# Performance work log

Hardware: AMD Instinct MI355X
Metric: run time of the kernel (lower is better)

The kernel has to match this reference:

```python
import jax, jax.numpy as jnp
import numpy as np

C = 64            # x_channel (d_model)
D = 2 * C         # d_inner (expand=2)
N = C // 2        # d_state
K = 4             # scan directions
R = -(-C // 16)   # dt_rank = ceil(d_model/16)
Bsz, H, W = 2, 48, 48
EPS = 1e-5


def setup_inputs() -> dict:
    key = jax.random.key(0)
    ks = jax.random.split(key, 8)
    g = lambda k, shp, s: jax.random.normal(k, shp, dtype=jnp.float32) * s
    return {
        "fufea1": g(ks[0], (Bsz, C, H, W), 1.0),
        "ln_g": jnp.ones((C,), jnp.float32),
        "ln_b": jnp.zeros((C,), jnp.float32),
        "in_proj_w": g(ks[1], (2 * D, C), C ** -0.5),
        "conv_w": g(ks[2], (D, 1, 3, 3), 1.0 / 3.0),   # depthwise 3x3
        "conv_b": g(ks[3], (D,), 0.02),
        "x_proj_w": g(ks[4], (K, R + 2 * N, D), D ** -0.5),
        "dt_w": g(ks[5], (K, D, R), R ** -0.5),
        "dt_b": g(ks[6], (K, D), 0.1),
        "A_logs": jnp.log(jnp.tile(jnp.arange(1, N + 1, dtype=jnp.float32), (K, D, 1))),  # S4D-real init
        "Ds": jnp.ones((K, D), jnp.float32),
        "out_ln_g": jnp.ones((D,), jnp.float32),
        "out_ln_b": jnp.zeros((D,), jnp.float32),
        "out_proj_w": g(ks[7], (C, D), D ** -0.5),
    }


def _layernorm(x, g, b):
    mu = x.mean(-1, keepdims=True)
    var = ((x - mu) ** 2).mean(-1, keepdims=True)
    return (x - mu) * jax.lax.rsqrt(var + EPS) * g + b


def reference(fufea1, ln_g, ln_b, in_proj_w, conv_w, conv_b, x_proj_w,
              dt_w, dt_b, A_logs, Ds, out_ln_g, out_ln_b, out_proj_w):
    B, Cc, Hh, Ww = fufea1.shape
    L = Hh * Ww
    # pre-LN (over channels, channels-last)
    xn = _layernorm(fufea1.transpose(0, 2, 3, 1), ln_g, ln_b)          # (B,H,W,C)
    # SS2D: in_proj -> split x,z
    xz = xn @ in_proj_w.T                                               # (B,H,W,2D)
    x, z = jnp.split(xz, 2, axis=-1)
    x = x.transpose(0, 3, 1, 2)                                         # (B,D,H,W)
    x = jax.lax.conv_general_dilated(x, conv_w, (1, 1), "SAME",
                                     feature_group_count=D,
                                     dimension_numbers=("NCHW", "OIHW", "NCHW"))
    x = jax.nn.silu(x + conv_b[None, :, None, None])
    # 4-direction sequences: row-major, col-major, and their reverses
    x_hw = x.reshape(B, D, L)
    x_wh = x.transpose(0, 1, 3, 2).reshape(B, D, L)
    xs = jnp.stack([x_hw, x_wh], axis=1)                                # (B,2,D,L)
    xs = jnp.concatenate([xs, jnp.flip(xs, axis=-1)], axis=1)           # (B,K,D,L)
    # per-direction projections of dt, B, C
    x_dbl = jnp.einsum("bkdl,kcd->bkcl", xs, x_proj_w)
    dts, Bs, Cs = jnp.split(x_dbl, [R, R + N], axis=2)                  # (B,K,R,L),(B,K,N,L),(B,K,N,L)
    dts = jnp.einsum("bkrl,kdr->bkdl", dts, dt_w)
    delta = jax.nn.softplus(dts + dt_b[None, :, :, None])               # (B,K,D,L)
    A = -jnp.exp(A_logs)                                                # (K,D,N)
    # selective scan over L; carry h: (B,K,D,N)
    u_l = xs.transpose(3, 0, 1, 2)                                      # (L,B,K,D)
    dt_l = delta.transpose(3, 0, 1, 2)
    B_l = Bs.transpose(3, 0, 1, 2)                                      # (L,B,K,N)
    C_l = Cs.transpose(3, 0, 1, 2)

    def step(h, inp):
        u_t, d_t, b_t, c_t = inp
        dA = jnp.exp(d_t[..., None] * A)                                # (B,K,D,N)
        h = dA * h + (d_t * u_t)[..., None] * b_t[:, :, None, :]
        y = jnp.einsum("bkdn,bkn->bkd", h, c_t)
        return h, y

    h0 = jnp.zeros((B, K, D, N), xs.dtype)
    _, ys = jax.lax.scan(step, h0, (u_l, dt_l, B_l, C_l))               # ys: (L,B,K,D)
    out_y = ys.transpose(1, 2, 3, 0) + Ds[None, :, :, None] * xs        # (B,K,D,L)
    # merge the 4 directions back to row-major hw order
    inv_y = jnp.flip(out_y[:, 2:4], axis=-1)                            # (B,2,D,L)
    wh = lambda t: t.reshape(B, D, Ww, Hh).transpose(0, 1, 3, 2).reshape(B, D, L)
    y = out_y[:, 0] + inv_y[:, 0] + wh(out_y[:, 1]) + wh(inv_y[:, 1])   # (B,D,L)
    y = y.transpose(0, 2, 1).reshape(B, Hh, Ww, D)
    y = _layernorm(y, out_ln_g, out_ln_b) * jax.nn.silu(z)
    out = (y @ out_proj_w.T).transpose(0, 3, 1, 2) + fufea1             # residual add
    return out
```

## Files before the change

kernel.cpp:

```cpp
#include <hip/hip_runtime.h>

#define Cc 64
#define Dd 128
#define Nn 32
#define Kk 4
#define Rr 4
#define Bb 2
#define Hh 48
#define Ww 48
#define Ll 2304
#define EPSf 1e-5f
#define LCc 144

#if __has_builtin(__builtin_amdgcn_exp2f)
#define EXP2F __builtin_amdgcn_exp2f
#else
#define EXP2F exp2f
#endif

__device__ __forceinline__ float wsum64(float v) {
  v += __shfl_xor(v, 32);
  v += __shfl_xor(v, 16);
  v += __shfl_xor(v, 8);
  v += __shfl_xor(v, 4);
  v += __shfl_xor(v, 2);
  v += __shfl_xor(v, 1);
  return v;
}

__global__ __launch_bounds__(256) void k1_ln_inproj(
    const float* __restrict__ x, const float* __restrict__ g,
    const float* __restrict__ bta, const float* __restrict__ Wp,
    float* __restrict__ xin, float* __restrict__ zb)
{
  __shared__ float xS[16][65];
  __shared__ float xnS[16][64];
  __shared__ float xaS[128][17];
  const int tid = threadIdx.x;
  const int wv = tid >> 6, lane = tid & 63;
  const int pbase = blockIdx.x * 16;
  const int b = pbase / Ll;
  const int lbase = pbase % Ll;
  {
    const int c = tid >> 2, li0 = (tid & 3) * 4;
    const float4 v4 = *(const float4*)&x[(b * Cc + c) * Ll + lbase + li0];
    xS[li0 + 0][c] = v4.x;
    xS[li0 + 1][c] = v4.y;
    xS[li0 + 2][c] = v4.z;
    xS[li0 + 3][c] = v4.w;
  }
  __syncthreads();
  const float gv = g[lane], bv = bta[lane];
  for (int pi = 0; pi < 4; ++pi) {
    const int p = wv * 4 + pi;
    const float v = xS[p][lane];
    const float mu = wsum64(v) * (1.0f / 64.0f);
    const float dv = v - mu;
    const float var = wsum64(dv * dv) * (1.0f / 64.0f);
    const float rs = rsqrtf(var + EPSf);
    xnS[p][lane] = dv * rs * gv + bv;
  }
  __syncthreads();
  float acc[4][4];
  #pragma unroll
  for (int pi = 0; pi < 4; ++pi)
    #pragma unroll
    for (int m = 0; m < 4; ++m) acc[pi][m] = 0.f;
  const float4* W4 = (const float4*)Wp;
  #pragma unroll 4
  for (int c4 = 0; c4 < 16; ++c4) {
    float4 xn4[4];
    #pragma unroll
    for (int pi = 0; pi < 4; ++pi)
      xn4[pi] = ((const float4*)xnS[wv * 4 + pi])[c4];
    #pragma unroll
    for (int m = 0; m < 4; ++m) {
      const float4 w4 = W4[(lane + 64 * m) * 16 + c4];
      #pragma unroll
      for (int pi = 0; pi < 4; ++pi)
        acc[pi][m] += xn4[pi].x * w4.x + xn4[pi].y * w4.y +
                      xn4[pi].z * w4.z + xn4[pi].w * w4.w;
    }
  }
  #pragma unroll
  for (int pi = 0; pi < 4; ++pi) {
    const int l = lbase + wv * 4 + pi;
    zb[(b * Ll + l) * Dd + lane]      = acc[pi][2];
    zb[(b * Ll + l) * Dd + lane + 64] = acc[pi][3];
    xaS[lane][wv * 4 + pi]      = acc[pi][0];
    xaS[lane + 64][wv * 4 + pi] = acc[pi][1];
  }
  __syncthreads();
  const int d = tid >> 1, off = (tid & 1) * 8;
  float* dst = &xin[(b * Dd + d) * Ll + lbase + off];
  #pragma unroll
  for (int i = 0; i < 8; ++i) dst[i] = xaS[d][off + i];
}

__global__ __launch_bounds__(512) void k3_proj(
    const float* __restrict__ xin, const float* __restrict__ cw,
    const float* __restrict__ cb, const float* __restrict__ xpw,
    const float* __restrict__ dtw, const float* __restrict__ dtb,
    float* __restrict__ xc, float2* __restrict__ dd2,
    float* __restrict__ Bm, float* __restrict__ Cm)
{
  __shared__ float xinS[128][30];
  __shared__ float xvS[8][132];
  __shared__ float dtsS[8][16];
  const int t = threadIdx.x;
  const int pb = blockIdx.x * 8;
  const int b = pb / Ll;
  const int lb = pb % Ll;
  const int h0 = lb / Ww, w0 = lb % Ww;
  for (int i = t; i < 3840; i += 512) {
    const int d = i / 30, j = i % 30;
    const int r = j / 10, c = j % 10;
    const int hh = h0 + r - 1, ww = w0 + c - 1;
    float v = 0.f;
    if (hh >= 0 && hh < Hh && ww >= 0 && ww < Ww)
      v = xin[(b * Dd + d) * Ll + hh * Ww + ww];
    xinS[d][j] = v;
  }
  __syncthreads();
  for (int i = t; i < 1024; i += 512) {
    const int pi = i >> 7, d = i & 127;
    float acc = cb[d];
    #pragma unroll
    for (int r = 0; r < 3; ++r)
      #pragma unroll
      for (int c = 0; c < 3; ++c)
        acc += xinS[d][r * 10 + pi + c] * cw[d * 9 + r * 3 + c];
    const float sig = 1.0f / (1.0f + __expf(-acc));
    xvS[pi][d] = acc * sig;
  }
  __syncthreads();
  for (int i = t; i < 1024; i += 512) {
    const int d = i >> 3, pi = i & 7;
    xc[(b * Dd + d) * Ll + lb + pi] = xvS[pi][d];
  }
  if (t < 272) {
    const int k = t / 68, c = t % 68;
    const size_t bkL = (size_t)(b * Kk + k) * Ll;
    float acc[8];
    #pragma unroll
    for (int pi = 0; pi < 8; ++pi) acc[pi] = 0.f;
    const float4* w4p = (const float4*)(xpw + (k * 68 + c) * 128);
    for (int d4 = 0; d4 < 32; ++d4) {
      const float4 w4 = w4p[d4];
      #pragma unroll
      for (int pi = 0; pi < 8; ++pi) {
        const float4 x4 = ((const float4*)xvS[pi])[d4];
        acc[pi] += x4.x * w4.x + x4.y * w4.y + x4.z * w4.z + x4.w * w4.w;
      }
    }
    #pragma unroll
    for (int pi = 0; pi < 8; ++pi) {
      const int l0 = lb + pi;
      const int h = l0 / Ww, w = l0 % Ww;
      int lk;
      if      (k == 0) lk = l0;
      else if (k == 1) lk = w * Hh + h;
      else if (k == 2) lk = Ll - 1 - l0;
      else             lk = Ll - 1 - (w * Hh + h);
      if (c < Rr)            dtsS[pi][k * 4 + c] = acc[pi];
      else if (c < Rr + Nn)  Bm[(bkL + lk) * Nn + (c - Rr)] = acc[pi];
      else                   Cm[(bkL + lk) * Nn + (c - Rr - Nn)] = acc[pi];
    }
  }
  __syncthreads();
  {
    const int k = t >> 7, dd = t & 127;
    const float4 dw = *(const float4*)&dtw[(k * Dd + dd) * 4];
    const float biasv = dtb[k * Dd + dd];
    float2* drow = dd2 + ((size_t)((b * Kk + k) * Dd) + dd) * Ll;
    float2 buf[8];
    #pragma unroll
    for (int pi = 0; pi < 8; ++pi) {
      const float a = biasv
          + dtsS[pi][k * 4 + 0] * dw.x + dtsS[pi][k * 4 + 1] * dw.y
          + dtsS[pi][k * 4 + 2] * dw.z + dtsS[pi][k * 4 + 3] * dw.w;
      const float sp = (a > 20.f) ? a : log1pf(__expf(a));
      buf[pi] = make_float2(sp, sp * xvS[pi][dd]);
    }
    if (k == 0) {
      float4* f4 = (float4*)(drow + lb);
      #pragma unroll
      for (int j = 0; j < 4; ++j)
        f4[j] = make_float4(buf[2 * j].x, buf[2 * j].y, buf[2 * j + 1].x, buf[2 * j + 1].y);
    } else if (k == 2) {
      float4* f4 = (float4*)(drow + (Ll - 8 - lb));
      #pragma unroll
      for (int j = 0; j < 4; ++j)
        f4[j] = make_float4(buf[7 - 2 * j].x, buf[7 - 2 * j].y, buf[6 - 2 * j].x, buf[6 - 2 * j].y);
    } else {
      #pragma unroll
      for (int pi = 0; pi < 8; ++pi) {
        const int l0 = lb + pi;
        const int h = l0 / Ww, w = l0 % Ww;
        int lk = w * Hh + h;
        if (k == 3) lk = Ll - 1 - lk;
        drow[lk] = buf[pi];
      }
    }
  }
}

__global__ __launch_bounds__(512) void k4_scan(
    const float2* __restrict__ dd2, const float* __restrict__ Bm,
    const float* __restrict__ Cm, const float* __restrict__ Alogs,
    float* __restrict__ ys)
{
  __shared__ float hendS[16][32];
  __shared__ float carryS[16][32];
  __shared__ float sumDS[16];
  __shared__ float pS[16][8][36];
  const int tid = threadIdx.x;
  const int s = tid >> 5, n = tid & 31;
  const int blk = blockIdx.x;
  const int d = blk & 127;
  const int k = (blk >> 7) & 3;
  const int b = blk >> 9;
  const float An = -__expf(Alogs[(k * Dd + d) * Nn + n]);
  const float AnE = An * 1.44269504f;
  const size_t bkL = (size_t)(b * Kk + k) * Ll;
  const float2* dP = dd2 + ((size_t)((b * Kk + k) * Dd) + d) * Ll;
  const float* bP = Bm + bkL * Nn + n;
  const float* cP = Cm + bkL * Nn + n;
  const int lbeg = s * LCc;
  float hA = 0.f, sumD = 0.f;
  {
    const float4* q4 = (const float4*)(dP + lbeg);
    const float* bl = bP + (size_t)lbeg * Nn;
    for (int it = 0; it < LCc / 4; ++it) {
      const float4 qa = q4[0], qb = q4[1]; q4 += 2;
      const float b0 = bl[0], b1 = bl[Nn], b2 = bl[2 * Nn], b3 = bl[3 * Nn];
      bl += 4 * Nn;
      hA = EXP2F(qa.x * AnE) * hA + qa.y * b0;
      hA = EXP2F(qa.z * AnE) * hA + qa.w * b1;
      hA = EXP2F(qb.x * AnE) * hA + qb.y * b2;
      hA = EXP2F(qb.z * AnE) * hA + qb.w * b3;
      sumD += (qa.x + qa.z) + (qb.x + qb.z);
    }
  }
  hendS[s][n] = hA;
  if (n == 0) sumDS[s] = sumD;
  __syncthreads();
  if (tid < 32) {
    float carry = 0.f;
    #pragma unroll
    for (int s2 = 0; s2 < 16; ++s2) {
      carryS[s2][tid] = carry;
      carry = EXP2F(AnE * sumDS[s2]) * carry + hendS[s2][tid];
    }
  }
  __syncthreads();
  float h = carryS[s][n];
  float* yP = ys + ((size_t)((b * Kk + k) * Dd) + d) * Ll + lbeg;
  const float4* q4 = (const float4*)(dP + lbeg);
  const float* bl = bP + (size_t)lbeg * Nn;
  const float* cl = cP + (size_t)lbeg * Nn;
  const int rrow = n & 7, qtr = n >> 3;
  for (int t8 = 0; t8 < LCc / 8; ++t8) {
    #pragma unroll
    for (int half = 0; half < 2; ++half) {
      const float4 qa = q4[0], qb = q4[1]; q4 += 2;
      const float b0 = bl[0], b1 = bl[Nn], b2 = bl[2 * Nn], b3 = bl[3 * Nn];
      const float c0 = cl[0], c1 = cl[Nn], c2 = cl[2 * Nn], c3 = cl[3 * Nn];
      bl += 4 * Nn; cl += 4 * Nn;
      h = EXP2F(qa.x * AnE) * h + qa.y * b0; pS[s][half * 4 + 0][n] = h * c0;
      h = EXP2F(qa.z * AnE) * h + qa.w * b1; pS[s][half * 4 + 1][n] = h * c1;
      h = EXP2F(qb.x * AnE) * h + qb.y * b2; pS[s][half * 4 + 2][n] = h * c2;
      h = EXP2F(qb.z * AnE) * h + qb.w * b3; pS[s][half * 4 + 3][n] = h * c3;
    }
    const float4 a4 = *(const float4*)&pS[s][rrow][qtr * 8];
    const float4 d4 = *(const float4*)&pS[s][rrow][qtr * 8 + 4];
    float sum = ((a4.x + a4.y) + (a4.z + a4.w)) + ((d4.x + d4.y) + (d4.z + d4.w));
    sum += __shfl_xor(sum, 8);
    sum += __shfl_xor(sum, 16);
    if (n < 8) yP[t8 * 8 + n] = sum;
  }
}

__global__ __launch_bounds__(256) void k5_merge(
    const float* __restrict__ ys, const float* __restrict__ zb,
    const float* __restrict__ og, const float* __restrict__ ob,
    const float* __restrict__ Wo, const float* __restrict__ resid,
    const float* __restrict__ xc, const float* __restrict__ DsP,
    float* __restrict__ out)
{
  __shared__ float ysS[4][16][128];
  __shared__ float tS[16][128];
  __shared__ float oS[64][17];
  __shared__ float xcS[16][128];
  const int tid = threadIdx.x;
  const int wv = tid >> 6, lane = tid & 63;
  const int pbase = blockIdx.x * 16;
  const int b = pbase / Ll;
  const int lbase = pbase % Ll;
  const int hrow = lbase / Ww, w0 = lbase % Ww;
  {
    const int dch = tid & 127, seg = tid >> 7;
    {
      const float4 a4 = *(const float4*)&xc[(b * Dd + dch) * Ll + lbase + seg * 8];
      const float4 c4 = *(const float4*)&xc[(b * Dd + dch) * Ll + lbase + seg * 8 + 4];
      xcS[seg * 8 + 0][dch] = a4.x; xcS[seg * 8 + 1][dch] = a4.y;
      xcS[seg * 8 + 2][dch] = a4.z; xcS[seg * 8 + 3][dch] = a4.w;
      xcS[seg * 8 + 4][dch] = c4.x; xcS[seg * 8 + 5][dch] = c4.y;
      xcS[seg * 8 + 6][dch] = c4.z; xcS[seg * 8 + 7][dch] = c4.w;
    }
    {
      const size_t r0 = ((size_t)(b * Kk + 0) * Dd + dch) * Ll + lbase + seg * 8;
      const float4 a4 = *(const float4*)&ys[r0];
      const float4 c4 = *(const float4*)&ys[r0 + 4];
      ysS[0][seg * 8 + 0][dch] = a4.x; ysS[0][seg * 8 + 1][dch] = a4.y;
      ysS[0][seg * 8 + 2][dch] = a4.z; ysS[0][seg * 8 + 3][dch] = a4.w;
      ysS[0][seg * 8 + 4][dch] = c4.x; ysS[0][seg * 8 + 5][dch] = c4.y;
      ysS[0][seg * 8 + 6][dch] = c4.z; ysS[0][seg * 8 + 7][dch] = c4.w;
    }
    {
      const size_t r2 = ((size_t)(b * Kk + 2) * Dd + dch) * Ll + (Ll - 16 - lbase) + seg * 8;
      const float4 a4 = *(const float4*)&ys[r2];
      const float4 c4 = *(const float4*)&ys[r2 + 4];
      ysS[2][15 - seg * 8 - 0][dch] = a4.x; ysS[2][15 - seg * 8 - 1][dch] = a4.y;
      ysS[2][15 - seg * 8 - 2][dch] = a4.z; ysS[2][15 - seg * 8 - 3][dch] = a4.w;
      ysS[2][15 - seg * 8 - 4][dch] = c4.x; ysS[2][15 - seg * 8 - 5][dch] = c4.y;
      ysS[2][15 - seg * 8 - 6][dch] = c4.z; ysS[2][15 - seg * 8 - 7][dch] = c4.w;
    }
    {
      const size_t r1 = ((size_t)(b * Kk + 1) * Dd + dch) * Ll;
      const size_t r3 = ((size_t)(b * Kk + 3) * Dd + dch) * Ll;
      #pragma unroll
      for (int j = 0; j < 8; ++j) {
        const int p = seg * 8 + j;
        const int l1 = (w0 + p) * Hh + hrow;
        ysS[1][p][dch] = ys[r1 + l1];
        ysS[3][p][dch] = ys[r3 + (Ll - 1 - l1)];
      }
    }
  }
  float sDs[2];
  #pragma unroll
  for (int m = 0; m < 2; ++m) {
    const int dch = lane + 64 * m;
    sDs[m] = DsP[dch] + DsP[Dd + dch] + DsP[2 * Dd + dch] + DsP[3 * Dd + dch];
  }
  __syncthreads();
  for (int pi = 0; pi < 4; ++pi) {
    const int p = wv * 4 + pi;
    const int l0 = lbase + p;
    float tv[2];
    #pragma unroll
    for (int m = 0; m < 2; ++m) {
      const int dch = lane + 64 * m;
      tv[m] = ysS[0][p][dch] + ysS[1][p][dch] + ysS[2][p][dch] + ysS[3][p][dch]
            + sDs[m] * xcS[p][dch];
    }
    const float mu = wsum64(tv[0] + tv[1]) * (1.0f / 128.0f);
    const float q = wsum64((tv[0] - mu) * (tv[0] - mu) +
                           (tv[1] - mu) * (tv[1] - mu)) * (1.0f / 128.0f);
    const float rs = rsqrtf(q + EPSf);
    #pragma unroll
    for (int m = 0; m < 2; ++m) {
      const int dch = lane + 64 * m;
      const float zz = zb[(size_t)(b * Ll + l0) * Dd + dch];
      const float sig = 1.0f / (1.0f + __expf(-zz));
      tS[p][dch] = ((tv[m] - mu) * rs * og[dch] + ob[dch]) * (zz * sig);
    }
  }
  __syncthreads();
  float acc[4] = {0.f, 0.f, 0.f, 0.f};
  const float4* W4 = (const float4*)Wo;
  for (int d4 = 0; d4 < 32; ++d4) {
    const float4 w4 = W4[lane * 32 + d4];
    #pragma unroll
    for (int pi = 0; pi < 4; ++pi) {
      const float4 t4 = ((const float4*)tS[wv * 4 + pi])[d4];
      acc[pi] += t4.x * w4.x + t4.y * w4.y + t4.z * w4.z + t4.w * w4.w;
    }
  }
  #pragma unroll
  for (int pi = 0; pi < 4; ++pi) oS[lane][wv * 4 + pi] = acc[pi];
  __syncthreads();
  const int c = tid >> 2, off = (tid & 3) * 4;
  const size_t obase = (size_t)(b * Cc + c) * Ll + lbase + off;
  const float4 r4 = *(const float4*)(resid + obase);
  float4 o4;
  o4.x = oS[c][off + 0] + r4.x;
  o4.y = oS[c][off + 1] + r4.y;
  o4.z = oS[c][off + 2] + r4.z;
  o4.w = oS[c][off + 3] + r4.w;
  *(float4*)(out + obase) = o4;
}

extern "C" void kernel_launch(void* const* d_in, const int* in_sizes, int n_in,
                              void* d_out, int out_size, void* d_ws, size_t ws_size,
                              hipStream_t stream)
{
  (void)in_sizes; (void)n_in; (void)out_size; (void)ws_size;
  const float* fufea1     = (const float*)d_in[0];
  const float* ln_g       = (const float*)d_in[1];
  const float* ln_b       = (const float*)d_in[2];
  const float* in_proj_w  = (const float*)d_in[3];
  const float* conv_w     = (const float*)d_in[4];
  const float* conv_b     = (const float*)d_in[5];
  const float* x_proj_w   = (const float*)d_in[6];
  const float* dt_w       = (const float*)d_in[7];
  const float* dt_b       = (const float*)d_in[8];
  const float* A_logs     = (const float*)d_in[9];
  const float* Ds         = (const float*)d_in[10];
  const float* out_ln_g   = (const float*)d_in[11];
  const float* out_ln_b   = (const float*)d_in[12];
  const float* out_proj_w = (const float*)d_in[13];

  float* ws  = (float*)d_ws;
  float* zb  = ws;
  float* xc  = ws + 589824;
  float* ysb = ws + 1179648;
  float* xin = ws + 1179648;
  float* Bm  = ws + 3538944;
  float* Cm  = ws + 4128768;
  float2* dd2 = (float2*)(ws + 4718592);

  k1_ln_inproj<<<288, 256, 0, stream>>>(fufea1, ln_g, ln_b, in_proj_w, xin, zb);
  k3_proj<<<576, 512, 0, stream>>>(xin, conv_w, conv_b, x_proj_w, dt_w, dt_b,
                                   xc, dd2, Bm, Cm);
  k4_scan<<<1024, 512, 0, stream>>>(dd2, Bm, Cm, A_logs, ysb);
  k5_merge<<<288, 256, 0, stream>>>(ysb, zb, out_ln_g, out_ln_b, out_proj_w, fufea1,
                                    xc, Ds, (float*)d_out);
}
```

Baseline: 220.3 us.

## Fuse LN+in_proj into conv/x_proj kernel, prefetch scan loads, remap scan blocks

Merges the layernorm/in_proj kernel into the depthwise-conv/x_proj kernel. Each block recomputes LN and the x half of in_proj for its 3x10 halo patch, which removes the xin round trip through global memory and one launch. The cost is roughly 3.75x redundant in_proj work on the x channels. The scan kernel now register-prefetches the next iteration's dt/B/C loads, and its block index is remapped so that consecutive blocks share d across b,k. The workspace layout is reorganised accordingly.

```diff
diff --git a/kernel.cpp b/kernel.cpp
--- a/kernel.cpp
+++ b/kernel.cpp
@@ -28,110 +28,97 @@
   return v;
 }
 
-__global__ __launch_bounds__(256) void k1_ln_inproj(
+__global__ __launch_bounds__(512) void k13(
     const float* __restrict__ x, const float* __restrict__ g,
     const float* __restrict__ bta, const float* __restrict__ Wp,
-    float* __restrict__ xin, float* __restrict__ zb)
+    const float* __restrict__ cw, const float* __restrict__ cb,
+    const float* __restrict__ xpw, const float* __restrict__ dtw,
+    const float* __restrict__ dtb,
+    float* __restrict__ zb, float* __restrict__ xc,
+    float2* __restrict__ dd2, float* __restrict__ Bm, float* __restrict__ Cm)
 {
-  __shared__ float xS[16][65];
-  __shared__ float xnS[16][64];
-  __shared__ float xaS[128][17];
-  const int tid = threadIdx.x;
-  const int wv = tid >> 6, lane = tid & 63;
-  const int pbase = blockIdx.x * 16;
-  const int b = pbase / Ll;
-  const int lbase = pbase % Ll;
-  {
-    const int c = tid >> 2, li0 = (tid & 3) * 4;
-    const float4 v4 = *(const float4*)&x[(b * Cc + c) * Ll + lbase + li0];
-    xS[li0 + 0][c] = v4.x;
-    xS[li0 + 1][c] = v4.y;
-    xS[li0 + 2][c] = v4.z;
-    xS[li0 + 3][c] = v4.w;
-  }
-  __syncthreads();
-  const float gv = g[lane], bv = bta[lane];
-  for (int pi = 0; pi < 4; ++pi) {
-    const int p = wv * 4 + pi;
-    const float v = xS[p][lane];
-    const float mu = wsum64(v) * (1.0f / 64.0f);
-    const float dv = v - mu;
-    const float var = wsum64(dv * dv) * (1.0f / 64.0f);
-    const float rs = rsqrtf(var + EPSf);
-    xnS[p][lane] = dv * rs * gv + bv;
-  }
-  __syncthreads();
-  float acc[4][4];
-  #pragma unroll
-  for (int pi = 0; pi < 4; ++pi)
-    #pragma unroll
-    for (int m = 0; m < 4; ++m) acc[pi][m] = 0.f;
-  const float4* W4 = (const float4*)Wp;
-  #pragma unroll 4
-  for (int c4 = 0; c4 < 16; ++c4) {
-    float4 xn4[4];
-    #pragma unroll
-    for (int pi = 0; pi < 4; ++pi)
-      xn4[pi] = ((const float4*)xnS[wv * 4 + pi])[c4];
-    #pragma unroll
-    for (int m = 0; m < 4; ++m) {
-      const float4 w4 = W4[(lane + 64 * m) * 16 + c4];
-      #pragma unroll
-      for (int pi = 0; pi < 4; ++pi)
-        acc[pi][m] += xn4[pi].x * w4.x + xn4[pi].y * w4.y +
-                      xn4[pi].z * w4.z + xn4[pi].w * w4.w;
-    }
-  }
-  #pragma unroll
-  for (int pi = 0; pi < 4; ++pi) {
-    const int l = lbase + wv * 4 + pi;
-    zb[(b * Ll + l) * Dd + lane]      = acc[pi][2];
-    zb[(b * Ll + l) * Dd + lane + 64] = acc[pi][3];
-    xaS[lane][wv * 4 + pi]      = acc[pi][0];
-    xaS[lane + 64][wv * 4 + pi] = acc[pi][1];
-  }
-  __syncthreads();
-  const int d = tid >> 1, off = (tid & 1) * 8;
-  float* dst = &xin[(b * Dd + d) * Ll + lbase + off];
-  #pragma unroll
-  for (int i = 0; i < 8; ++i) dst[i] = xaS[d][off + i];
-}
-
-__global__ __launch_bounds__(512) void k3_proj(
-    const float* __restrict__ xin, const float* __restrict__ cw,
-    const float* __restrict__ cb, const float* __restrict__ xpw,
-    const float* __restrict__ dtw, const float* __restrict__ dtb,
-    float* __restrict__ xc, float2* __restrict__ dd2,
-    float* __restrict__ Bm, float* __restrict__ Cm)
-{
-  __shared__ float xinS[128][30];
+  __shared__ float xnS[30][68];
+  __shared__ float xpS[30][132];
   __shared__ float xvS[8][132];
   __shared__ float dtsS[8][16];
   const int t = threadIdx.x;
+  const int wv = t >> 6, lane = t & 63;
   const int pb = blockIdx.x * 8;
   const int b = pb / Ll;
   const int lb = pb % Ll;
   const int h0 = lb / Ww, w0 = lb % Ww;
-  for (int i = t; i < 3840; i += 512) {
-    const int d = i / 30, j = i % 30;
-    const int r = j / 10, c = j % 10;
-    const int hh = h0 + r - 1, ww = w0 + c - 1;
-    float v = 0.f;
-    if (hh >= 0 && hh < Hh && ww >= 0 && ww < Ww)
-      v = xin[(b * Dd + d) * Ll + hh * Ww + ww];
-    xinS[d][j] = v;
-  }
-  __syncthreads();
-  for (int i = t; i < 1024; i += 512) {
-    const int pi = i >> 7, d = i & 127;
-    float acc = cb[d];
+  {
+    const int c = t >> 3, q = t & 7;
+    #pragma unroll
+    for (int it = 0; it < 4; ++it) {
+      const int p = it * 8 + q;
+      if (p < 30) {
+        const int r = p / 10, ccol = p % 10;
+        const int hh = h0 + r - 1, ww2 = w0 + ccol - 1;
+        float v = 0.f;
+        if (hh >= 0 && hh < Hh && ww2 >= 0 && ww2 < Ww)
+          v = x[(b * Cc + c) * Ll + hh * Ww + ww2];
+        xnS[p][c] = v;
+      }
+    }
+  }
+  __syncthreads();
+  {
+    const float gv = g[lane], bv = bta[lane];
+    #pragma unroll
+    for (int it = 0; it < 4; ++it) {
+      const int p = it * 8 + wv;
+      if (p < 30) {
+        const float v = xnS[p][lane];
+        const float mu = wsum64(v) * (1.0f / 64.0f);
+        const float dv = v - mu;
+        const float var = wsum64(dv * dv) * (1.0f / 64.0f);
+        const float rs = rsqrtf(var + EPSf);
+        xnS[p][lane] = dv * rs * gv + bv;
+      }
+    }
+  }
+  __syncthreads();
+  for (int o = t; o < 3840; o += 512) {
+    const int p = o >> 7, dch = o & 127;
+    const int r = p / 10, ccol = p % 10;
+    const int hh = h0 + r - 1, ww2 = w0 + ccol - 1;
+    float acc = 0.f;
+    if (hh >= 0 && hh < Hh && ww2 >= 0 && ww2 < Ww) {
+      const float4* wr = (const float4*)(Wp + dch * 64);
+      #pragma unroll 4
+      for (int c4 = 0; c4 < 16; ++c4) {
+        const float4 w4 = wr[c4];
+        const float4 x4 = *(const float4*)&xnS[p][c4 * 4];
+        acc += x4.x * w4.x + x4.y * w4.y + x4.z * w4.z + x4.w * w4.w;
+      }
+    }
+    xpS[p][dch] = acc;
+  }
+  for (int o = t; o < 1024; o += 512) {
+    const int pi = o >> 7, dch = o & 127;
+    const int p = 11 + pi;
+    const float4* wr = (const float4*)(Wp + (128 + dch) * 64);
+    float acc = 0.f;
+    #pragma unroll 4
+    for (int c4 = 0; c4 < 16; ++c4) {
+      const float4 w4 = wr[c4];
+      const float4 x4 = *(const float4*)&xnS[p][c4 * 4];
+      acc += x4.x * w4.x + x4.y * w4.y + x4.z * w4.z + x4.w * w4.w;
+    }
+    zb[(size_t)(b * Ll + lb + pi) * Dd + dch] = acc;
+  }
+  __syncthreads();
+  for (int o = t; o < 1024; o += 512) {
+    const int pi = o >> 7, dch = o & 127;
+    float acc = cb[dch];
     #pragma unroll
     for (int r = 0; r < 3; ++r)
       #pragma unroll
       for (int c = 0; c < 3; ++c)
-        acc += xinS[d][r * 10 + pi + c] * cw[d * 9 + r * 3 + c];
+        acc += xpS[r * 10 + pi + c][dch] * cw[dch * 9 + r * 3 + c];
     const float sig = 1.0f / (1.0f + __expf(-acc));
-    xvS[pi][d] = acc * sig;
+    xvS[pi][dch] = acc * sig;
   }
   __syncthreads();
   for (int i = t; i < 1024; i += 512) {
@@ -217,9 +204,9 @@
   const int tid = threadIdx.x;
   const int s = tid >> 5, n = tid & 31;
   const int blk = blockIdx.x;
-  const int d = blk & 127;
-  const int k = (blk >> 7) & 3;
-  const int b = blk >> 9;
+  const int bk = blk & 7;
+  const int d = blk >> 3;
+  const int b = bk >> 2, k = bk & 3;
   const float An = -__expf(Alogs[(k * Dd + d) * Nn + n]);
   const float AnE = An * 1.44269504f;
   const size_t bkL = (size_t)(b * Kk + k) * Ll;
@@ -231,15 +218,18 @@
   {
     const float4* q4 = (const float4*)(dP + lbeg);
     const float* bl = bP + (size_t)lbeg * Nn;
+    float4 qa = q4[0], qb = q4[1];
+    float b0 = bl[0], b1 = bl[Nn], b2 = bl[2 * Nn], b3 = bl[3 * Nn];
     for (int it = 0; it < LCc / 4; ++it) {
-      const float4 qa = q4[0], qb = q4[1]; q4 += 2;
-      const float b0 = bl[0], b1 = bl[Nn], b2 = bl[2 * Nn], b3 = bl[3 * Nn];
-      bl += 4 * Nn;
+      q4 += 2; bl += 4 * Nn;
+      const float4 qa_n = q4[0], qb_n = q4[1];
+      const float b0n = bl[0], b1n = bl[Nn], b2n = bl[2 * Nn], b3n = bl[3 * Nn];
       hA = EXP2F(qa.x * AnE) * hA + qa.y * b0;
       hA = EXP2F(qa.z * AnE) * hA + qa.w * b1;
       hA = EXP2F(qb.x * AnE) * hA + qb.y * b2;
       hA = EXP2F(qb.z * AnE) * hA + qb.w * b3;
       sumD += (qa.x + qa.z) + (qb.x + qb.z);
+      qa = qa_n; qb = qb_n; b0 = b0n; b1 = b1n; b2 = b2n; b3 = b3n;
     }
   }
   hendS[s][n] = hA;
@@ -260,17 +250,22 @@
   const float* bl = bP + (size_t)lbeg * Nn;
   const float* cl = cP + (size_t)lbeg * Nn;
   const int rrow = n & 7, qtr = n >> 3;
+  float4 qa = q4[0], qb = q4[1];
+  float b0 = bl[0], b1 = bl[Nn], b2 = bl[2 * Nn], b3 = bl[3 * Nn];
+  float c0 = cl[0], c1 = cl[Nn], c2 = cl[2 * Nn], c3 = cl[3 * Nn];
   for (int t8 = 0; t8 < LCc / 8; ++t8) {
     #pragma unroll
     for (int half = 0; half < 2; ++half) {
-      const float4 qa = q4[0], qb = q4[1]; q4 += 2;
-      const float b0 = bl[0], b1 = bl[Nn], b2 = bl[2 * Nn], b3 = bl[3 * Nn];
-      const float c0 = cl[0], c1 = cl[Nn], c2 = cl[2 * Nn], c3 = cl[3 * Nn];
-      bl += 4 * Nn; cl += 4 * Nn;
+      q4 += 2; bl += 4 * Nn; cl += 4 * Nn;
+      const float4 qa_n = q4[0], qb_n = q4[1];
+      const float b0n = bl[0], b1n = bl[Nn], b2n = bl[2 * Nn], b3n = bl[3 * Nn];
+      const float c0n = cl[0], c1n = cl[Nn], c2n = cl[2 * Nn], c3n = cl[3 * Nn];
       h = EXP2F(qa.x * AnE) * h + qa.y * b0; pS[s][half * 4 + 0][n] = h * c0;
       h = EXP2F(qa.z * AnE) * h + qa.w * b1; pS[s][half * 4 + 1][n] = h * c1;
       h = EXP2F(qb.x * AnE) * h + qb.y * b2; pS[s][half * 4 + 2][n] = h * c2;
       h = EXP2F(qb.z * AnE) * h + qb.w * b3; pS[s][half * 4 + 3][n] = h * c3;
+      qa = qa_n; qb = qb_n; b0 = b0n; b1 = b1n; b2 = b2n; b3 = b3n;
+      c0 = c0n; c1 = c1n; c2 = c2n; c3 = c3n;
     }
     const float4 a4 = *(const float4*)&pS[s][rrow][qtr * 8];
     const float4 d4 = *(const float4*)&pS[s][rrow][qtr * 8 + 4];
@@ -412,18 +407,16 @@
   const float* out_ln_b   = (const float*)d_in[12];
   const float* out_proj_w = (const float*)d_in[13];
 
-  float* ws  = (float*)d_ws;
-  float* zb  = ws;
-  float* xc  = ws + 589824;
-  float* ysb = ws + 1179648;
-  float* xin = ws + 1179648;
-  float* Bm  = ws + 3538944;
-  float* Cm  = ws + 4128768;
-  float2* dd2 = (float2*)(ws + 4718592);
-
-  k1_ln_inproj<<<288, 256, 0, stream>>>(fufea1, ln_g, ln_b, in_proj_w, xin, zb);
-  k3_proj<<<576, 512, 0, stream>>>(xin, conv_w, conv_b, x_proj_w, dt_w, dt_b,
-                                   xc, dd2, Bm, Cm);
+  float* ws = (float*)d_ws;
+  float2* dd2 = (float2*)ws;
+  float* Bm   = ws + 4718592;
+  float* Cm   = ws + 5308416;
+  float* zb   = ws + 5898240;
+  float* xc   = ws + 6488064;
+  float* ysb  = ws + 7077888;
+
+  k13<<<576, 512, 0, stream>>>(fufea1, ln_g, ln_b, in_proj_w, conv_w, conv_b,
+                               x_proj_w, dt_w, dt_b, zb, xc, dd2, Bm, Cm);
   k4_scan<<<1024, 512, 0, stream>>>(dd2, Bm, Cm, A_logs, ysb);
   k5_merge<<<288, 256, 0, stream>>>(ysb, zb, out_ln_g, out_ln_b, out_proj_w, fufea1,
                                     xc, Ds, (float*)d_out);
```

Measured after the change: 296.7 us. 34.7% more time.

## Software-prefetch scan inputs, reorder scan block mapping, and relocate workspace buffers

Applied to the files above, without the earlier changes.

The scan kernel now loads the next step's delta/B/C values one iteration ahead so global memory latency overlaps the serial recurrence. Block indices are remapped so consecutive blocks cover all 8 (b,k) pairs for the same d. That lets neighbouring blocks share the same B/C rows in cache rather than all 128 d for one (b,k) in sequence. The workspace layout is also reordered, putting dd2 first. Prefetching raises register pressure and reads one element past each chunk on the last iteration. That overread stays inside the allocated buffer.

```diff
diff --git a/kernel.cpp b/kernel.cpp
--- a/kernel.cpp
+++ b/kernel.cpp
@@ -217,9 +217,9 @@
   const int tid = threadIdx.x;
   const int s = tid >> 5, n = tid & 31;
   const int blk = blockIdx.x;
-  const int d = blk & 127;
-  const int k = (blk >> 7) & 3;
-  const int b = blk >> 9;
+  const int bk = blk & 7;
+  const int d = blk >> 3;
+  const int b = bk >> 2, k = bk & 3;
   const float An = -__expf(Alogs[(k * Dd + d) * Nn + n]);
   const float AnE = An * 1.44269504f;
   const size_t bkL = (size_t)(b * Kk + k) * Ll;
@@ -231,15 +231,18 @@
   {
     const float4* q4 = (const float4*)(dP + lbeg);
     const float* bl = bP + (size_t)lbeg * Nn;
+    float4 qa = q4[0], qb = q4[1];
+    float b0 = bl[0], b1 = bl[Nn], b2 = bl[2 * Nn], b3 = bl[3 * Nn];
     for (int it = 0; it < LCc / 4; ++it) {
-      const float4 qa = q4[0], qb = q4[1]; q4 += 2;
-      const float b0 = bl[0], b1 = bl[Nn], b2 = bl[2 * Nn], b3 = bl[3 * Nn];
-      bl += 4 * Nn;
+      q4 += 2; bl += 4 * Nn;
+      const float4 qa_n = q4[0], qb_n = q4[1];
+      const float b0n = bl[0], b1n = bl[Nn], b2n = bl[2 * Nn], b3n = bl[3 * Nn];
       hA = EXP2F(qa.x * AnE) * hA + qa.y * b0;
       hA = EXP2F(qa.z * AnE) * hA + qa.w * b1;
       hA = EXP2F(qb.x * AnE) * hA + qb.y * b2;
       hA = EXP2F(qb.z * AnE) * hA + qb.w * b3;
       sumD += (qa.x + qa.z) + (qb.x + qb.z);
+      qa = qa_n; qb = qb_n; b0 = b0n; b1 = b1n; b2 = b2n; b3 = b3n;
     }
   }
   hendS[s][n] = hA;
@@ -260,17 +263,22 @@
   const float* bl = bP + (size_t)lbeg * Nn;
   const float* cl = cP + (size_t)lbeg * Nn;
   const int rrow = n & 7, qtr = n >> 3;
+  float4 qa = q4[0], qb = q4[1];
+  float b0 = bl[0], b1 = bl[Nn], b2 = bl[2 * Nn], b3 = bl[3 * Nn];
+  float c0 = cl[0], c1 = cl[Nn], c2 = cl[2 * Nn], c3 = cl[3 * Nn];
   for (int t8 = 0; t8 < LCc / 8; ++t8) {
     #pragma unroll
     for (int half = 0; half < 2; ++half) {
-      const float4 qa = q4[0], qb = q4[1]; q4 += 2;
-      const float b0 = bl[0], b1 = bl[Nn], b2 = bl[2 * Nn], b3 = bl[3 * Nn];
-      const float c0 = cl[0], c1 = cl[Nn], c2 = cl[2 * Nn], c3 = cl[3 * Nn];
-      bl += 4 * Nn; cl += 4 * Nn;
+      q4 += 2; bl += 4 * Nn; cl += 4 * Nn;
+      const float4 qa_n = q4[0], qb_n = q4[1];
+      const float b0n = bl[0], b1n = bl[Nn], b2n = bl[2 * Nn], b3n = bl[3 * Nn];
+      const float c0n = cl[0], c1n = cl[Nn], c2n = cl[2 * Nn], c3n = cl[3 * Nn];
       h = EXP2F(qa.x * AnE) * h + qa.y * b0; pS[s][half * 4 + 0][n] = h * c0;
       h = EXP2F(qa.z * AnE) * h + qa.w * b1; pS[s][half * 4 + 1][n] = h * c1;
       h = EXP2F(qb.x * AnE) * h + qb.y * b2; pS[s][half * 4 + 2][n] = h * c2;
       h = EXP2F(qb.z * AnE) * h + qb.w * b3; pS[s][half * 4 + 3][n] = h * c3;
+      qa = qa_n; qb = qb_n; b0 = b0n; b1 = b1n; b2 = b2n; b3 = b3n;
+      c0 = c0n; c1 = c1n; c2 = c2n; c3 = c3n;
     }
     const float4 a4 = *(const float4*)&pS[s][rrow][qtr * 8];
     const float4 d4 = *(const float4*)&pS[s][rrow][qtr * 8 + 4];
@@ -412,14 +420,14 @@
   const float* out_ln_b   = (const float*)d_in[12];
   const float* out_proj_w = (const float*)d_in[13];
 
-  float* ws  = (float*)d_ws;
-  float* zb  = ws;
-  float* xc  = ws + 589824;
-  float* ysb = ws + 1179648;
-  float* xin = ws + 1179648;
-  float* Bm  = ws + 3538944;
-  float* Cm  = ws + 4128768;
-  float2* dd2 = (float2*)(ws + 4718592);
+  float* ws = (float*)d_ws;
+  float2* dd2 = (float2*)ws;
+  float* Bm   = ws + 4718592;
+  float* Cm   = ws + 5308416;
+  float* zb   = ws + 5898240;
+  float* xc   = ws + 6488064;
+  float* ysb  = ws + 7077888;
+  float* xin  = ws + 7077888;
 
   k1_ln_inproj<<<288, 256, 0, stream>>>(fufea1, ln_g, ln_b, in_proj_w, xin, zb);
   k3_proj<<<576, 512, 0, stream>>>(xin, conv_w, conv_b, x_proj_w, dt_w, dt_b,
```

Result: no change. 219.6 us, median of 2 (-0.3%).
